# Kernel tuning notes

Measured on AMD Instinct MI355X. Metric: run time of the kernel, lower is better.

The kernel has to match this reference:

```python
import jax, jax.numpy as jnp
import numpy as np

DIN = 256
HID = 512

def setup_inputs() -> dict:
    key = jax.random.key(0)
    ks = jax.random.split(key, 9)
    s_in = 1.0 / np.sqrt(DIN)
    s_h = 1.0 / np.sqrt(HID)
    h = jax.random.normal(ks[0], (32, 1024, DIN), dtype=jnp.float32)
    Wv = jax.random.uniform(ks[1], (HID, DIN), jnp.float32, -s_in, s_in)
    bv = jax.random.uniform(ks[2], (HID,), jnp.float32, -s_in, s_in)
    Wk = jax.random.uniform(ks[3], (HID, DIN), jnp.float32, -s_in, s_in)
    bk = jax.random.uniform(ks[4], (HID,), jnp.float32, -s_in, s_in)
    Wq = jax.random.uniform(ks[5], (HID, DIN), jnp.float32, -s_in, s_in)
    bq = jax.random.uniform(ks[6], (HID,), jnp.float32, -s_in, s_in)
    Wo = jax.random.uniform(ks[7], (DIN, HID), jnp.float32, -s_h, s_h)
    bo = jax.random.uniform(ks[8], (DIN,), jnp.float32, -s_h, s_h)
    return {"h": h, "Wv": Wv, "bv": bv, "Wk": Wk, "bk": bk, "Wq": Wq, "bq": bq, "Wo": Wo, "bo": bo}

def reference(h, Wv, bv, Wk, bk, Wq, bq, Wo, bo):
    # relu-activated Q/K/V projections: [B, N, HID]
    v = jax.nn.relu(jnp.einsum('bnd,hd->bnh', h, Wv) + bv)
    q = jax.nn.relu(jnp.einsum('bnd,hd->bnh', h, Wq) + bq)
    k = jax.nn.relu(jnp.einsum('bnd,hd->bnh', h, Wk) + bk)
    # unscaled attention: [B, N, N]
    att = jax.nn.softmax(jnp.einsum('bnh,bmh->bnm', q, k), axis=2)
    out = jnp.einsum('bnm,bmh->bnh', att, v)          # [B, N, HID]
    out = jax.nn.relu(jnp.einsum('bnh,dh->bnd', out, Wo) + bo)  # [B, N, DIN]
    return out
```

## Files before the change

kernel.cpp:

```cpp
#include <hip/hip_runtime.h>
#include <cstdint>
#include <cstddef>

#define NB    32
#define SEQ   1024
#define DIN   256
#define HID   512
#define MTOT  32768

typedef _Float16 half_t;
typedef _Float16 half8  __attribute__((ext_vector_type(8)));
typedef _Float16 half4v __attribute__((ext_vector_type(4)));
typedef float    f32x4  __attribute__((ext_vector_type(4)));

typedef __attribute__((address_space(1))) const void* gas_ptr;
typedef __attribute__((address_space(3))) void*       las_ptr;

__global__ void cvt_kernel(const float* __restrict__ src, half_t* __restrict__ dst, int n4) {
    int i = blockIdx.x * blockDim.x + threadIdx.x;
    if (i < n4) {
        f32x4 v = ((const f32x4*)src)[i];
        half4v h;
        h[0] = (half_t)v[0]; h[1] = (half_t)v[1]; h[2] = (half_t)v[2]; h[3] = (half_t)v[3];
        ((half4v*)dst)[i] = h;
    }
}

__global__ void pack_bias(const float* __restrict__ bv, const float* __restrict__ bk,
                          const float* __restrict__ bq, float* __restrict__ dst) {
    int t = threadIdx.x;
    if (t < HID) {
        dst[t]         = bv[t];
        dst[HID + t]   = bk[t];
        dst[2*HID + t] = bq[t];
    }
}

template<int MODE>
__global__ __launch_bounds__(256, 2) void gemm_k(
    const half_t* __restrict__ A, long lda, long a_bs,
    const half_t* __restrict__ Bw, long ldb, long b_bs,
    void* __restrict__ Out, long ldo, long o_bs,
    const float* __restrict__ bias,
    int Kdim, half_t* __restrict__ out2)
{
    __shared__ alignas(16) half_t As[128 * 32];
    __shared__ alignas(16) half_t Bs[128 * 32];

    const int t    = threadIdx.x;
    const int lane = t & 63;
    const int wave = t >> 6;
    const int wm   = wave >> 1;
    const int wn   = wave & 1;
    const int lanen = lane & 15;
    const int quad  = lane >> 4;
    const int z     = blockIdx.z;
    const long m0 = (long)blockIdx.x * 128;
    const long n0 = (long)blockIdx.y * 128;

    const half_t* Ab = A  + (long)z * a_bs;
    const half_t* Bb = Bw + (long)z * b_bs;

    f32x4 acc[4][4];
#pragma unroll
    for (int i = 0; i < 4; i++)
#pragma unroll
        for (int j = 0; j < 4; j++)
            acc[i][j] = f32x4{0.f, 0.f, 0.f, 0.f};

    const int c0 = t, c1 = t + 256;
    const int r0 = c0 >> 2, kc0 = c0 & 3;
    const int r1 = c1 >> 2, kc1 = c1 & 3;

    const half_t* gA0 = Ab + (m0 + r0) * lda + kc0 * 8;
    const half_t* gA1 = Ab + (m0 + r1) * lda + kc1 * 8;
    const half_t* gB0 = Bb + (n0 + r0) * ldb + kc0 * 8;
    const half_t* gB1 = Bb + (n0 + r1) * ldb + kc1 * 8;
    half_t* lA0 = &As[c0 * 8];
    half_t* lA1 = &As[c1 * 8];
    half_t* lB0 = &Bs[c0 * 8];
    half_t* lB1 = &Bs[c1 * 8];

    int aoff[4], boff[4];
#pragma unroll
    for (int i = 0; i < 4; i++) aoff[i] = (wm * 64 + i * 16 + lanen) * 32 + quad * 8;
#pragma unroll
    for (int j = 0; j < 4; j++) boff[j] = (wn * 64 + j * 16 + lanen) * 32 + quad * 8;

    for (int k0 = 0; k0 < Kdim; k0 += 32) {
        __builtin_amdgcn_global_load_lds((gas_ptr)(gA0 + k0), (las_ptr)lA0, 16, 0, 0);
        __builtin_amdgcn_global_load_lds((gas_ptr)(gA1 + k0), (las_ptr)lA1, 16, 0, 0);
        __builtin_amdgcn_global_load_lds((gas_ptr)(gB0 + k0), (las_ptr)lB0, 16, 0, 0);
        __builtin_amdgcn_global_load_lds((gas_ptr)(gB1 + k0), (las_ptr)lB1, 16, 0, 0);
        __syncthreads();

        half8 af[4], bf[4];
#pragma unroll
        for (int i = 0; i < 4; i++) af[i] = *(const half8*)&As[aoff[i]];
#pragma unroll
        for (int j = 0; j < 4; j++) bf[j] = *(const half8*)&Bs[boff[j]];
#pragma unroll
        for (int i = 0; i < 4; i++)
#pragma unroll
            for (int j = 0; j < 4; j++)
                acc[i][j] = __builtin_amdgcn_mfma_f32_16x16x32_f16(af[i], bf[j], acc[i][j], 0, 0, 0);
        __syncthreads();
    }

#pragma unroll
    for (int i = 0; i < 4; i++) {
        long mrow = m0 + wm * 64 + i * 16 + quad * 4;
#pragma unroll
        for (int j = 0; j < 4; j++) {
            long gn = n0 + wn * 64 + j * 16 + lanen;
            f32x4 v = acc[i][j];
            if (MODE == 0) {
                float bb = bias[z * HID + gn];
                half_t h0 = (half_t)fmaxf(v[0] + bb, 0.f);
                half_t h1 = (half_t)fmaxf(v[1] + bb, 0.f);
                half_t h2 = (half_t)fmaxf(v[2] + bb, 0.f);
                half_t h3 = (half_t)fmaxf(v[3] + bb, 0.f);
                if (z == 0) {
                    long bidx = mrow >> 10;
                    long pos  = mrow & 1023;
                    half4v pk; pk[0] = h0; pk[1] = h1; pk[2] = h2; pk[3] = h3;
                    *(half4v*)(out2 + ((bidx * HID + gn) << 10) + pos) = pk;
                } else {
                    half_t* o = (half_t*)Out + (long)(z - 1) * o_bs;
                    o[(mrow + 0) * ldo + gn] = h0;
                    o[(mrow + 1) * ldo + gn] = h1;
                    o[(mrow + 2) * ldo + gn] = h2;
                    o[(mrow + 3) * ldo + gn] = h3;
                }
            } else {
                float* o = (float*)Out;
                float bb = bias[gn];
#pragma unroll
                for (int r = 0; r < 4; r++) o[(mrow + r) * ldo + gn] = fmaxf(v[r] + bb, 0.f);
            }
        }
    }
}

__global__ __launch_bounds__(256, 2) void se_k(
    const half_t* __restrict__ Q, const half_t* __restrict__ K,
    half_t* __restrict__ E, float* __restrict__ Mstat, float* __restrict__ Lstat)
{
    __shared__ alignas(16) half_t As[128 * 32];
    __shared__ alignas(16) half_t Bs[128 * 32];
    __shared__ float redM[2][128];
    __shared__ float redL[2][128];

    const int t    = threadIdx.x;
    const int lane = t & 63;
    const int wave = t >> 6;
    const int wm   = wave >> 1;
    const int wn   = wave & 1;
    const int lanen = lane & 15;
    const int quad  = lane >> 4;
    const int z     = blockIdx.z;
    const int kb    = blockIdx.y;
    const long m0 = (long)blockIdx.x * 128;
    const long n0 = (long)kb * 128;

    const half_t* Ab = Q + (long)z * SEQ * HID;
    const half_t* Bb = K + (long)z * SEQ * HID;

    f32x4 acc[4][4];
#pragma unroll
    for (int i = 0; i < 4; i++)
#pragma unroll
        for (int j = 0; j < 4; j++)
            acc[i][j] = f32x4{0.f, 0.f, 0.f, 0.f};

    const int c0 = t, c1 = t + 256;
    const int r0 = c0 >> 2, kc0 = c0 & 3;
    const int r1 = c1 >> 2, kc1 = c1 & 3;

    const half_t* gA0 = Ab + (m0 + r0) * HID + kc0 * 8;
    const half_t* gA1 = Ab + (m0 + r1) * HID + kc1 * 8;
    const half_t* gB0 = Bb + (n0 + r0) * HID + kc0 * 8;
    const half_t* gB1 = Bb + (n0 + r1) * HID + kc1 * 8;
    half_t* lA0 = &As[c0 * 8];
    half_t* lA1 = &As[c1 * 8];
    half_t* lB0 = &Bs[c0 * 8];
    half_t* lB1 = &Bs[c1 * 8];

    int aoff[4], boff[4];
#pragma unroll
    for (int i = 0; i < 4; i++) aoff[i] = (wm * 64 + i * 16 + lanen) * 32 + quad * 8;
#pragma unroll
    for (int j = 0; j < 4; j++) boff[j] = (wn * 64 + j * 16 + lanen) * 32 + quad * 8;

    for (int k0 = 0; k0 < HID; k0 += 32) {
        __builtin_amdgcn_global_load_lds((gas_ptr)(gA0 + k0), (las_ptr)lA0, 16, 0, 0);
        __builtin_amdgcn_global_load_lds((gas_ptr)(gA1 + k0), (las_ptr)lA1, 16, 0, 0);
        __builtin_amdgcn_global_load_lds((gas_ptr)(gB0 + k0), (las_ptr)lB0, 16, 0, 0);
        __builtin_amdgcn_global_load_lds((gas_ptr)(gB1 + k0), (las_ptr)lB1, 16, 0, 0);
        __syncthreads();

        half8 af[4], bf[4];
#pragma unroll
        for (int i = 0; i < 4; i++) af[i] = *(const half8*)&As[aoff[i]];
#pragma unroll
        for (int j = 0; j < 4; j++) bf[j] = *(const half8*)&Bs[boff[j]];
#pragma unroll
        for (int i = 0; i < 4; i++)
#pragma unroll
            for (int j = 0; j < 4; j++)
                acc[i][j] = __builtin_amdgcn_mfma_f32_16x16x32_f16(af[i], bf[j], acc[i][j], 0, 0, 0);
        __syncthreads();
    }

    float rm[4][4];
#pragma unroll
    for (int i = 0; i < 4; i++)
#pragma unroll
        for (int r = 0; r < 4; r++) {
            float v = fmaxf(fmaxf(acc[i][0][r], acc[i][1][r]), fmaxf(acc[i][2][r], acc[i][3][r]));
#pragma unroll
            for (int off = 8; off > 0; off >>= 1)
                v = fmaxf(v, __shfl_xor(v, off, 64));
            rm[i][r] = v;
        }
    if (lanen == 0) {
#pragma unroll
        for (int i = 0; i < 4; i++)
#pragma unroll
            for (int r = 0; r < 4; r++)
                redM[wn][wm * 64 + i * 16 + quad * 4 + r] = rm[i][r];
    }
    __syncthreads();

    float mf[4][4];
#pragma unroll
    for (int i = 0; i < 4; i++)
#pragma unroll
        for (int r = 0; r < 4; r++) {
            int rl = wm * 64 + i * 16 + quad * 4 + r;
            mf[i][r] = fmaxf(redM[0][rl], redM[1][rl]);
        }

    half_t* Eb = E + (long)z * SEQ * SEQ;
    float rs[4][4];
#pragma unroll
    for (int i = 0; i < 4; i++)
#pragma unroll
        for (int r = 0; r < 4; r++) rs[i][r] = 0.f;
#pragma unroll
    for (int i = 0; i < 4; i++) {
        long mrow = m0 + wm * 64 + i * 16 + quad * 4;
#pragma unroll
        for (int j = 0; j < 4; j++) {
            long gn = n0 + wn * 64 + j * 16 + lanen;
#pragma unroll
            for (int r = 0; r < 4; r++) {
                float e = __expf(acc[i][j][r] - mf[i][r]);
                rs[i][r] += e;
                Eb[(mrow + r) * SEQ + gn] = (half_t)e;
            }
        }
    }
#pragma unroll
    for (int i = 0; i < 4; i++)
#pragma unroll
        for (int r = 0; r < 4; r++) {
            float v = rs[i][r];
#pragma unroll
            for (int off = 8; off > 0; off >>= 1)
                v += __shfl_xor(v, off, 64);
            rs[i][r] = v;
        }
    if (lanen == 0) {
#pragma unroll
        for (int i = 0; i < 4; i++)
#pragma unroll
            for (int r = 0; r < 4; r++)
                redL[wn][wm * 64 + i * 16 + quad * 4 + r] = rs[i][r];
    }
    __syncthreads();

    if (t < 128) {
        long sidx = ((long)z * 8 + kb) * SEQ + m0 + t;
        Mstat[sidx] = fmaxf(redM[0][t], redM[1][t]);
        Lstat[sidx] = redL[0][t] + redL[1][t];
    }
}

__global__ __launch_bounds__(256, 2) void pv_k(
    const half_t* __restrict__ E, const half_t* __restrict__ vT,
    const float* __restrict__ Mstat, const float* __restrict__ Lstat,
    half_t* __restrict__ O16)
{
    __shared__ alignas(16) half_t As[128 * 32];
    __shared__ alignas(16) half_t Bs[128 * 32];
    __shared__ float scaleS[8][128];
    __shared__ float invS[128];

    const int t    = threadIdx.x;
    const int lane = t & 63;
    const int wave = t >> 6;
    const int wm   = wave >> 1;
    const int wn   = wave & 1;
    const int lanen = lane & 15;
    const int quad  = lane >> 4;
    const int z     = blockIdx.z;
    const long m0 = (long)blockIdx.x * 128;
    const long h0 = (long)blockIdx.y * 128;

    if (t < 128) {
        float mv[8];
        float M = -1e30f;
#pragma unroll
        for (int kb = 0; kb < 8; kb++) {
            mv[kb] = Mstat[((long)z * 8 + kb) * SEQ + m0 + t];
            M = fmaxf(M, mv[kb]);
        }
        float ls = 0.f;
#pragma unroll
        for (int kb = 0; kb < 8; kb++) {
            float sc = __expf(mv[kb] - M);
            scaleS[kb][t] = sc;
            ls += Lstat[((long)z * 8 + kb) * SEQ + m0 + t] * sc;
        }
        invS[t] = 1.f / ls;
    }
    __syncthreads();

    const half_t* Ab = E  + (long)z * SEQ * SEQ;
    const half_t* Bb = vT + (long)z * HID * SEQ;

    f32x4 acc[4][4];
#pragma unroll
    for (int i = 0; i < 4; i++)
#pragma unroll
        for (int j = 0; j < 4; j++)
            acc[i][j] = f32x4{0.f, 0.f, 0.f, 0.f};

    const int c0 = t, c1 = t + 256;
    const int r0 = c0 >> 2, kc0 = c0 & 3;
    const int r1 = c1 >> 2, kc1 = c1 & 3;

    const half_t* gA0 = Ab + (m0 + r0) * SEQ + kc0 * 8;
    const half_t* gA1 = Ab + (m0 + r1) * SEQ + kc1 * 8;
    const half_t* gB0 = Bb + (h0 + r0) * SEQ + kc0 * 8;
    const half_t* gB1 = Bb + (h0 + r1) * SEQ + kc1 * 8;
    half_t* lA0 = &As[c0 * 8];
    half_t* lA1 = &As[c1 * 8];
    half_t* lB0 = &Bs[c0 * 8];
    half_t* lB1 = &Bs[c1 * 8];

    int aoff[4], boff[4];
#pragma unroll
    for (int i = 0; i < 4; i++) aoff[i] = (wm * 64 + i * 16 + lanen) * 32 + quad * 8;
#pragma unroll
    for (int j = 0; j < 4; j++) boff[j] = (wn * 64 + j * 16 + lanen) * 32 + quad * 8;

    for (int k0 = 0; k0 < SEQ; k0 += 32) {
        __builtin_amdgcn_global_load_lds((gas_ptr)(gA0 + k0), (las_ptr)lA0, 16, 0, 0);
        __builtin_amdgcn_global_load_lds((gas_ptr)(gA1 + k0), (las_ptr)lA1, 16, 0, 0);
        __builtin_amdgcn_global_load_lds((gas_ptr)(gB0 + k0), (las_ptr)lB0, 16, 0, 0);
        __builtin_amdgcn_global_load_lds((gas_ptr)(gB1 + k0), (las_ptr)lB1, 16, 0, 0);
        __syncthreads();

        const int kb = k0 >> 7;
        half8 af[4], bf[4];
#pragma unroll
        for (int i = 0; i < 4; i++) {
            af[i] = *(const half8*)&As[aoff[i]];
            half_t sh = (half_t)scaleS[kb][wm * 64 + i * 16 + lanen];
            af[i] *= sh;
        }
#pragma unroll
        for (int j = 0; j < 4; j++) bf[j] = *(const half8*)&Bs[boff[j]];
#pragma unroll
        for (int i = 0; i < 4; i++)
#pragma unroll
            for (int j = 0; j < 4; j++)
                acc[i][j] = __builtin_amdgcn_mfma_f32_16x16x32_f16(af[i], bf[j], acc[i][j], 0, 0, 0);
        __syncthreads();
    }

    half_t* o = O16 + (long)z * SEQ * HID;
#pragma unroll
    for (int i = 0; i < 4; i++) {
        long mrow = m0 + wm * 64 + i * 16 + quad * 4;
        int rl = wm * 64 + i * 16 + quad * 4;
#pragma unroll
        for (int j = 0; j < 4; j++) {
            long gn = h0 + wn * 64 + j * 16 + lanen;
#pragma unroll
            for (int r = 0; r < 4; r++)
                o[(mrow + r) * HID + gn] = (half_t)(acc[i][j][r] * invS[rl + r]);
        }
    }
}

extern "C" void kernel_launch(void* const* d_in, const int* in_sizes, int n_in,
                              void* d_out, int out_size, void* d_ws, size_t ws_size,
                              hipStream_t stream) {
    const float* h  = (const float*)d_in[0];
    const float* Wv = (const float*)d_in[1];
    const float* bv = (const float*)d_in[2];
    const float* Wk = (const float*)d_in[3];
    const float* bk = (const float*)d_in[4];
    const float* Wq = (const float*)d_in[5];
    const float* bq = (const float*)d_in[6];
    const float* Wo = (const float*)d_in[7];
    const float* bo = (const float*)d_in[8];

    uint8_t* ws = (uint8_t*)d_ws;
    size_t off = 0;
    auto alloc = [&](size_t bytes) { size_t o = off; off += (bytes + 255) & ~(size_t)255; return o; };

    half_t* W16   = (half_t*)(ws + alloc((size_t)3 * HID * DIN * 2));
    half_t* Wo16  = (half_t*)(ws + alloc((size_t)DIN * HID * 2));
    float*  biasq = (float*)(ws + alloc((size_t)3 * HID * 4));
    half_t* k16   = (half_t*)(ws + alloc((size_t)MTOT * HID * 2));
    half_t* q16   = (half_t*)(ws + alloc((size_t)MTOT * HID * 2));
    half_t* vT    = (half_t*)(ws + alloc((size_t)MTOT * HID * 2));
    size_t h16_off = alloc((size_t)MTOT * DIN * 2);
    half_t* h16   = (half_t*)(ws + h16_off);
    half_t* O16 = q16;

    size_t s_avail = ws_size > h16_off ? ws_size - h16_off : 0;
    size_t per_batch = (size_t)SEQ * SEQ * 2 + 2 * 8 * SEQ * 4;
    int GB = (int)(s_avail / per_batch);
    if (GB < 1)  GB = 1;
    if (GB > NB) GB = NB;
    half_t* Ebuf  = (half_t*)(ws + h16_off);
    float*  Mstat = (float*)(ws + h16_off + (size_t)GB * SEQ * SEQ * 2);
    float*  Lstat = Mstat + (size_t)GB * 8 * SEQ;

    cvt_kernel<<<dim3((MTOT * DIN / 4 + 255) / 256), 256, 0, stream>>>(h, h16, MTOT * DIN / 4);
    cvt_kernel<<<dim3((HID * DIN / 4 + 255) / 256), 256, 0, stream>>>(Wv, W16, HID * DIN / 4);
    cvt_kernel<<<dim3((HID * DIN / 4 + 255) / 256), 256, 0, stream>>>(Wk, W16 + HID * DIN, HID * DIN / 4);
    cvt_kernel<<<dim3((HID * DIN / 4 + 255) / 256), 256, 0, stream>>>(Wq, W16 + 2 * HID * DIN, HID * DIN / 4);
    cvt_kernel<<<dim3((DIN * HID / 4 + 255) / 256), 256, 0, stream>>>(Wo, Wo16, DIN * HID / 4);
    pack_bias<<<dim3(1), 512, 0, stream>>>(bv, bk, bq, biasq);

    gemm_k<0><<<dim3(MTOT / 128, HID / 128, 3), 256, 0, stream>>>(
        h16, DIN, 0,
        W16, DIN, (long)HID * DIN,
        (void*)k16, HID, (long)MTOT * HID,
        biasq, DIN, vT);

    for (int g0 = 0; g0 < NB; g0 += GB) {
        int gb = NB - g0 < GB ? NB - g0 : GB;
        se_k<<<dim3(SEQ / 128, SEQ / 128, gb), 256, 0, stream>>>(
            q16 + (size_t)g0 * SEQ * HID,
            k16 + (size_t)g0 * SEQ * HID,
            Ebuf, Mstat, Lstat);
        pv_k<<<dim3(SEQ / 128, HID / 128, gb), 256, 0, stream>>>(
            Ebuf, vT + (size_t)g0 * HID * SEQ,
            Mstat, Lstat,
            O16 + (size_t)g0 * SEQ * HID);
    }

    gemm_k<3><<<dim3(MTOT / 128, DIN / 128, 1), 256, 0, stream>>>(
        O16, HID, 0,
        Wo16, HID, 0,
        d_out, DIN, 0,
        bo, HID, nullptr);

    (void)in_sizes; (void)n_in; (void)out_size;
}
```

Measured before the change: 302.0 us.

## Widen attention tiles to 128x256 and merge weight conversions into one launch

The score-exp kernel and the PV kernel now compute 128x256 output tiles per block instead of 128x128. Each wave holds 4x8 MFMA accumulators, which halves the grid and reloads each A tile half as often. In se_k the cross-wave LDS max/sum reduction is removed: each wave writes its own 128-column partial statistics directly into the existing 8 slots per row. The four weight fp32-to-fp16 conversions are merged into a single launch indexed by blockIdx.y. The larger accumulator arrays raise register pressure and may hurt occupancy under launch_bounds(256,2).

```diff
diff --git a/kernel.cpp b/kernel.cpp
--- a/kernel.cpp
+++ b/kernel.cpp
@@ -23,6 +23,22 @@
         half4v h;
         h[0] = (half_t)v[0]; h[1] = (half_t)v[1]; h[2] = (half_t)v[2]; h[3] = (half_t)v[3];
         ((half4v*)dst)[i] = h;
+    }
+}
+
+__global__ void cvt4_kernel(const float* __restrict__ s0, const float* __restrict__ s1,
+                            const float* __restrict__ s2, const float* __restrict__ s3,
+                            half_t* __restrict__ d0, half_t* __restrict__ d1,
+                            half_t* __restrict__ d2, half_t* __restrict__ d3, int n4) {
+    int y = blockIdx.y;
+    const float* s = y == 0 ? s0 : y == 1 ? s1 : y == 2 ? s2 : s3;
+    half_t*      d = y == 0 ? d0 : y == 1 ? d1 : y == 2 ? d2 : d3;
+    int i = blockIdx.x * blockDim.x + threadIdx.x;
+    if (i < n4) {
+        f32x4 v = ((const f32x4*)s)[i];
+        half4v h;
+        h[0] = (half_t)v[0]; h[1] = (half_t)v[1]; h[2] = (half_t)v[2]; h[3] = (half_t)v[3];
+        ((half4v*)d)[i] = h;
     }
 }
 
@@ -147,155 +163,7 @@
     half_t* __restrict__ E, float* __restrict__ Mstat, float* __restrict__ Lstat)
 {
     __shared__ alignas(16) half_t As[128 * 32];
-    __shared__ alignas(16) half_t Bs[128 * 32];
-    __shared__ float redM[2][128];
-    __shared__ float redL[2][128];
-
-    const int t    = threadIdx.x;
-    const int lane = t & 63;
-    const int wave = t >> 6;
-    const int wm   = wave >> 1;
-    const int wn   = wave & 1;
-    const int lanen = lane & 15;
-    const int quad  = lane >> 4;
-    const int z     = blockIdx.z;
-    const int kb    = blockIdx.y;
-    const long m0 = (long)blockIdx.x * 128;
-    const long n0 = (long)kb * 128;
-
-    const half_t* Ab = Q + (long)z * SEQ * HID;
-    const half_t* Bb = K + (long)z * SEQ * HID;
-
-    f32x4 acc[4][4];
-#pragma unroll
-    for (int i = 0; i < 4; i++)
-#pragma unroll
-        for (int j = 0; j < 4; j++)
-            acc[i][j] = f32x4{0.f, 0.f, 0.f, 0.f};
-
-    const int c0 = t, c1 = t + 256;
-    const int r0 = c0 >> 2, kc0 = c0 & 3;
-    const int r1 = c1 >> 2, kc1 = c1 & 3;
-
-    const half_t* gA0 = Ab + (m0 + r0) * HID + kc0 * 8;
-    const half_t* gA1 = Ab + (m0 + r1) * HID + kc1 * 8;
-    const half_t* gB0 = Bb + (n0 + r0) * HID + kc0 * 8;
-    const half_t* gB1 = Bb + (n0 + r1) * HID + kc1 * 8;
-    half_t* lA0 = &As[c0 * 8];
-    half_t* lA1 = &As[c1 * 8];
-    half_t* lB0 = &Bs[c0 * 8];
-    half_t* lB1 = &Bs[c1 * 8];
-
-    int aoff[4], boff[4];
-#pragma unroll
-    for (int i = 0; i < 4; i++) aoff[i] = (wm * 64 + i * 16 + lanen) * 32 + quad * 8;
-#pragma unroll
-    for (int j = 0; j < 4; j++) boff[j] = (wn * 64 + j * 16 + lanen) * 32 + quad * 8;
-
-    for (int k0 = 0; k0 < HID; k0 += 32) {
-        __builtin_amdgcn_global_load_lds((gas_ptr)(gA0 + k0), (las_ptr)lA0, 16, 0, 0);
-        __builtin_amdgcn_global_load_lds((gas_ptr)(gA1 + k0), (las_ptr)lA1, 16, 0, 0);
-        __builtin_amdgcn_global_load_lds((gas_ptr)(gB0 + k0), (las_ptr)lB0, 16, 0, 0);
-        __builtin_amdgcn_global_load_lds((gas_ptr)(gB1 + k0), (las_ptr)lB1, 16, 0, 0);
-        __syncthreads();
-
-        half8 af[4], bf[4];
-#pragma unroll
-        for (int i = 0; i < 4; i++) af[i] = *(const half8*)&As[aoff[i]];
-#pragma unroll
-        for (int j = 0; j < 4; j++) bf[j] = *(const half8*)&Bs[boff[j]];
-#pragma unroll
-        for (int i = 0; i < 4; i++)
-#pragma unroll
-            for (int j = 0; j < 4; j++)
-                acc[i][j] = __builtin_amdgcn_mfma_f32_16x16x32_f16(af[i], bf[j], acc[i][j], 0, 0, 0);
-        __syncthreads();
-    }
-
-    float rm[4][4];
-#pragma unroll
-    for (int i = 0; i < 4; i++)
-#pragma unroll
-        for (int r = 0; r < 4; r++) {
-            float v = fmaxf(fmaxf(acc[i][0][r], acc[i][1][r]), fmaxf(acc[i][2][r], acc[i][3][r]));
-#pragma unroll
-            for (int off = 8; off > 0; off >>= 1)
-                v = fmaxf(v, __shfl_xor(v, off, 64));
-            rm[i][r] = v;
-        }
-    if (lanen == 0) {
-#pragma unroll
-        for (int i = 0; i < 4; i++)
-#pragma unroll
-            for (int r = 0; r < 4; r++)
-                redM[wn][wm * 64 + i * 16 + quad * 4 + r] = rm[i][r];
-    }
-    __syncthreads();
-
-    float mf[4][4];
-#pragma unroll
-    for (int i = 0; i < 4; i++)
-#pragma unroll
-        for (int r = 0; r < 4; r++) {
-            int rl = wm * 64 + i * 16 + quad * 4 + r;
-            mf[i][r] = fmaxf(redM[0][rl], redM[1][rl]);
-        }
-
-    half_t* Eb = E + (long)z * SEQ * SEQ;
-    float rs[4][4];
-#pragma unroll
-    for (int i = 0; i < 4; i++)
-#pragma unroll
-        for (int r = 0; r < 4; r++) rs[i][r] = 0.f;
-#pragma unroll
-    for (int i = 0; i < 4; i++) {
-        long mrow = m0 + wm * 64 + i * 16 + quad * 4;
-#pragma unroll
-        for (int j = 0; j < 4; j++) {
-            long gn = n0 + wn * 64 + j * 16 + lanen;
-#pragma unroll
-            for (int r = 0; r < 4; r++) {
-                float e = __expf(acc[i][j][r] - mf[i][r]);
-                rs[i][r] += e;
-                Eb[(mrow + r) * SEQ + gn] = (half_t)e;
-            }
-        }
-    }
-#pragma unroll
-    for (int i = 0; i < 4; i++)
-#pragma unroll
-        for (int r = 0; r < 4; r++) {
-            float v = rs[i][r];
-#pragma unroll
-            for (int off = 8; off > 0; off >>= 1)
-                v += __shfl_xor(v, off, 64);
-            rs[i][r] = v;
-        }
-    if (lanen == 0) {
-#pragma unroll
-        for (int i = 0; i < 4; i++)
-#pragma unroll
-            for (int r = 0; r < 4; r++)
-                redL[wn][wm * 64 + i * 16 + quad * 4 + r] = rs[i][r];
-    }
-    __syncthreads();
-
-    if (t < 128) {
-        long sidx = ((long)z * 8 + kb) * SEQ + m0 + t;
-        Mstat[sidx] = fmaxf(redM[0][t], redM[1][t]);
-        Lstat[sidx] = redL[0][t] + redL[1][t];
-    }
-}
-
-__global__ __launch_bounds__(256, 2) void pv_k(
-    const half_t* __restrict__ E, const half_t* __restrict__ vT,
-    const float* __restrict__ Mstat, const float* __restrict__ Lstat,
-    half_t* __restrict__ O16)
-{
-    __shared__ alignas(16) half_t As[128 * 32];
-    __shared__ alignas(16) half_t Bs[128 * 32];
-    __shared__ float scaleS[8][128];
-    __shared__ float invS[128];
+    __shared__ alignas(16) half_t Bs[256 * 32];
 
     const int t    = threadIdx.x;
     const int lane = t & 63;
@@ -306,7 +174,138 @@
     const int quad  = lane >> 4;
     const int z     = blockIdx.z;
     const long m0 = (long)blockIdx.x * 128;
-    const long h0 = (long)blockIdx.y * 128;
+    const long n0 = (long)blockIdx.y * 256;
+
+    const half_t* Ab = Q + (long)z * SEQ * HID;
+    const half_t* Bb = K + (long)z * SEQ * HID;
+
+    f32x4 acc[4][8];
+#pragma unroll
+    for (int i = 0; i < 4; i++)
+#pragma unroll
+        for (int j = 0; j < 8; j++)
+            acc[i][j] = f32x4{0.f, 0.f, 0.f, 0.f};
+
+    const half_t* gA[2]; half_t* lA[2];
+    const half_t* gB[4]; half_t* lB[4];
+#pragma unroll
+    for (int s = 0; s < 2; s++) {
+        int c = t + 256 * s;
+        gA[s] = Ab + (m0 + (c >> 2)) * HID + (c & 3) * 8;
+        lA[s] = &As[c * 8];
+    }
+#pragma unroll
+    for (int s = 0; s < 4; s++) {
+        int c = t + 256 * s;
+        gB[s] = Bb + (n0 + (c >> 2)) * HID + (c & 3) * 8;
+        lB[s] = &Bs[c * 8];
+    }
+
+    int aoff[4], boff[8];
+#pragma unroll
+    for (int i = 0; i < 4; i++) aoff[i] = (wm * 64 + i * 16 + lanen) * 32 + quad * 8;
+#pragma unroll
+    for (int j = 0; j < 8; j++) boff[j] = (wn * 128 + j * 16 + lanen) * 32 + quad * 8;
+
+    for (int k0 = 0; k0 < HID; k0 += 32) {
+#pragma unroll
+        for (int s = 0; s < 2; s++)
+            __builtin_amdgcn_global_load_lds((gas_ptr)(gA[s] + k0), (las_ptr)lA[s], 16, 0, 0);
+#pragma unroll
+        for (int s = 0; s < 4; s++)
+            __builtin_amdgcn_global_load_lds((gas_ptr)(gB[s] + k0), (las_ptr)lB[s], 16, 0, 0);
+        __syncthreads();
+
+        half8 af[4], bf[8];
+#pragma unroll
+        for (int i = 0; i < 4; i++) af[i] = *(const half8*)&As[aoff[i]];
+#pragma unroll
+        for (int j = 0; j < 8; j++) bf[j] = *(const half8*)&Bs[boff[j]];
+#pragma unroll
+        for (int i = 0; i < 4; i++)
+#pragma unroll
+            for (int j = 0; j < 8; j++)
+                acc[i][j] = __builtin_amdgcn_mfma_f32_16x16x32_f16(af[i], bf[j], acc[i][j], 0, 0, 0);
+        __syncthreads();
+    }
+
+    float mf[4][4];
+#pragma unroll
+    for (int i = 0; i < 4; i++)
+#pragma unroll
+        for (int r = 0; r < 4; r++) {
+            float v = acc[i][0][r];
+#pragma unroll
+            for (int j = 1; j < 8; j++) v = fmaxf(v, acc[i][j][r]);
+#pragma unroll
+            for (int off = 8; off > 0; off >>= 1)
+                v = fmaxf(v, __shfl_xor(v, off, 64));
+            mf[i][r] = v;
+        }
+
+    half_t* Eb = E + (long)z * SEQ * SEQ;
+    float rs[4][4];
+#pragma unroll
+    for (int i = 0; i < 4; i++)
+#pragma unroll
+        for (int r = 0; r < 4; r++) rs[i][r] = 0.f;
+#pragma unroll
+    for (int i = 0; i < 4; i++) {
+        long mrow = m0 + wm * 64 + i * 16 + quad * 4;
+#pragma unroll
+        for (int j = 0; j < 8; j++) {
+            long gn = n0 + wn * 128 + j * 16 + lanen;
+#pragma unroll
+            for (int r = 0; r < 4; r++) {
+                float e = __expf(acc[i][j][r] - mf[i][r]);
+                rs[i][r] += e;
+                Eb[(mrow + r) * SEQ + gn] = (half_t)e;
+            }
+        }
+    }
+#pragma unroll
+    for (int i = 0; i < 4; i++)
+#pragma unroll
+        for (int r = 0; r < 4; r++) {
+            float v = rs[i][r];
+#pragma unroll
+            for (int off = 8; off > 0; off >>= 1)
+                v += __shfl_xor(v, off, 64);
+            rs[i][r] = v;
+        }
+
+    if (lanen == 0) {
+        long base = ((long)z * 8 + blockIdx.y * 2 + wn) * SEQ + m0 + wm * 64;
+#pragma unroll
+        for (int i = 0; i < 4; i++)
+#pragma unroll
+            for (int r = 0; r < 4; r++) {
+                Mstat[base + i * 16 + quad * 4 + r] = mf[i][r];
+                Lstat[base + i * 16 + quad * 4 + r] = rs[i][r];
+            }
+    }
+}
+
+__global__ __launch_bounds__(256, 2) void pv_k(
+    const half_t* __restrict__ E, const half_t* __restrict__ vT,
+    const float* __restrict__ Mstat, const float* __restrict__ Lstat,
+    half_t* __restrict__ O16)
+{
+    __shared__ alignas(16) half_t As[128 * 32];
+    __shared__ alignas(16) half_t Bs[256 * 32];
+    __shared__ float scaleS[8][128];
+    __shared__ float invS[128];
+
+    const int t    = threadIdx.x;
+    const int lane = t & 63;
+    const int wave = t >> 6;
+    const int wm   = wave >> 1;
+    const int wn   = wave & 1;
+    const int lanen = lane & 15;
+    const int quad  = lane >> 4;
+    const int z     = blockIdx.z;
+    const long m0 = (long)blockIdx.x * 128;
+    const long h0 = (long)blockIdx.y * 256;
 
     if (t < 128) {
         float mv[8];
@@ -330,41 +329,45 @@
     const half_t* Ab = E  + (long)z * SEQ * SEQ;
     const half_t* Bb = vT + (long)z * HID * SEQ;
 
-    f32x4 acc[4][4];
-#pragma unroll
-    for (int i = 0; i < 4; i++)
-#pragma unroll
-        for (int j = 0; j < 4; j++)
+    f32x4 acc[4][8];
+#pragma unroll
+    for (int i = 0; i < 4; i++)
+#pragma unroll
+        for (int j = 0; j < 8; j++)
             acc[i][j] = f32x4{0.f, 0.f, 0.f, 0.f};
 
-    const int c0 = t, c1 = t + 256;
-    const int r0 = c0 >> 2, kc0 = c0 & 3;
-    const int r1 = c1 >> 2, kc1 = c1 & 3;
-
-    const half_t* gA0 = Ab + (m0 + r0) * SEQ + kc0 * 8;
-    const half_t* gA1 = Ab + (m0 + r1) * SEQ + kc1 * 8;
-    const half_t* gB0 = Bb + (h0 + r0) * SEQ + kc0 * 8;
-    const half_t* gB1 = Bb + (h0 + r1) * SEQ + kc1 * 8;
-    half_t* lA0 = &As[c0 * 8];
-    half_t* lA1 = &As[c1 * 8];
-    half_t* lB0 = &Bs[c0 * 8];
-    half_t* lB1 = &Bs[c1 * 8];
-
-    int aoff[4], boff[4];
+    const half_t* gA[2]; half_t* lA[2];
+    const half_t* gB[4]; half_t* lB[4];
+#pragma unroll
+    for (int s = 0; s < 2; s++) {
+        int c = t + 256 * s;
+        gA[s] = Ab + (m0 + (c >> 2)) * SEQ + (c & 3) * 8;
+        lA[s] = &As[c * 8];
+    }
+#pragma unroll
+    for (int s = 0; s < 4; s++) {
+        int c = t + 256 * s;
+        gB[s] = Bb + (h0 + (c >> 2)) * SEQ + (c & 3) * 8;
+        lB[s] = &Bs[c * 8];
+    }
+
+    int aoff[4], boff[8];
 #pragma unroll
     for (int i = 0; i < 4; i++) aoff[i] = (wm * 64 + i * 16 + lanen) * 32 + quad * 8;
 #pragma unroll
-    for (int j = 0; j < 4; j++) boff[j] = (wn * 64 + j * 16 + lanen) * 32 + quad * 8;
+    for (int j = 0; j < 8; j++) boff[j] = (wn * 128 + j * 16 + lanen) * 32 + quad * 8;
 
     for (int k0 = 0; k0 < SEQ; k0 += 32) {
-        __builtin_amdgcn_global_load_lds((gas_ptr)(gA0 + k0), (las_ptr)lA0, 16, 0, 0);
-        __builtin_amdgcn_global_load_lds((gas_ptr)(gA1 + k0), (las_ptr)lA1, 16, 0, 0);
-        __builtin_amdgcn_global_load_lds((gas_ptr)(gB0 + k0), (las_ptr)lB0, 16, 0, 0);
-        __builtin_amdgcn_global_load_lds((gas_ptr)(gB1 + k0), (las_ptr)lB1, 16, 0, 0);
+#pragma unroll
+        for (int s = 0; s < 2; s++)
+            __builtin_amdgcn_global_load_lds((gas_ptr)(gA[s] + k0), (las_ptr)lA[s], 16, 0, 0);
+#pragma unroll
+        for (int s = 0; s < 4; s++)
+            __builtin_amdgcn_global_load_lds((gas_ptr)(gB[s] + k0), (las_ptr)lB[s], 16, 0, 0);
         __syncthreads();
 
         const int kb = k0 >> 7;
-        half8 af[4], bf[4];
+        half8 af[4], bf[8];
 #pragma unroll
         for (int i = 0; i < 4; i++) {
             af[i] = *(const half8*)&As[aoff[i]];
@@ -372,11 +375,11 @@
             af[i] *= sh;
         }
 #pragma unroll
-        for (int j = 0; j < 4; j++) bf[j] = *(const half8*)&Bs[boff[j]];
+        for (int j = 0; j < 8; j++) bf[j] = *(const half8*)&Bs[boff[j]];
 #pragma unroll
         for (int i = 0; i < 4; i++)
 #pragma unroll
-            for (int j = 0; j < 4; j++)
+            for (int j = 0; j < 8; j++)
                 acc[i][j] = __builtin_amdgcn_mfma_f32_16x16x32_f16(af[i], bf[j], acc[i][j], 0, 0, 0);
         __syncthreads();
     }
@@ -387,8 +390,8 @@
         long mrow = m0 + wm * 64 + i * 16 + quad * 4;
         int rl = wm * 64 + i * 16 + quad * 4;
 #pragma unroll
-        for (int j = 0; j < 4; j++) {
-            long gn = h0 + wn * 64 + j * 16 + lanen;
+        for (int j = 0; j < 8; j++) {
+            long gn = h0 + wn * 128 + j * 16 + lanen;
 #pragma unroll
             for (int r = 0; r < 4; r++)
                 o[(mrow + r) * HID + gn] = (half_t)(acc[i][j][r] * invS[rl + r]);
@@ -433,10 +436,8 @@
     float*  Lstat = Mstat + (size_t)GB * 8 * SEQ;
 
     cvt_kernel<<<dim3((MTOT * DIN / 4 + 255) / 256), 256, 0, stream>>>(h, h16, MTOT * DIN / 4);
-    cvt_kernel<<<dim3((HID * DIN / 4 + 255) / 256), 256, 0, stream>>>(Wv, W16, HID * DIN / 4);
-    cvt_kernel<<<dim3((HID * DIN / 4 + 255) / 256), 256, 0, stream>>>(Wk, W16 + HID * DIN, HID * DIN / 4);
-    cvt_kernel<<<dim3((HID * DIN / 4 + 255) / 256), 256, 0, stream>>>(Wq, W16 + 2 * HID * DIN, HID * DIN / 4);
-    cvt_kernel<<<dim3((DIN * HID / 4 + 255) / 256), 256, 0, stream>>>(Wo, Wo16, DIN * HID / 4);
+    cvt4_kernel<<<dim3((HID * DIN / 4 + 255) / 256, 4), 256, 0, stream>>>(
+        Wv, Wk, Wq, Wo, W16, W16 + HID * DIN, W16 + 2 * HID * DIN, Wo16, HID * DIN / 4);
     pack_bias<<<dim3(1), 512, 0, stream>>>(bv, bk, bq, biasq);
 
     gemm_k<0><<<dim3(MTOT / 128, HID / 128, 3), 256, 0, stream>>>(
@@ -447,11 +448,11 @@
 
     for (int g0 = 0; g0 < NB; g0 += GB) {
         int gb = NB - g0 < GB ? NB - g0 : GB;
-        se_k<<<dim3(SEQ / 128, SEQ / 128, gb), 256, 0, stream>>>(
+        se_k<<<dim3(SEQ / 128, SEQ / 256, gb), 256, 0, stream>>>(
             q16 + (size_t)g0 * SEQ * HID,
             k16 + (size_t)g0 * SEQ * HID,
             Ebuf, Mstat, Lstat);
-        pv_k<<<dim3(SEQ / 128, HID / 128, gb), 256, 0, stream>>>(
+        pv_k<<<dim3(SEQ / 128, HID / 256, gb), 256, 0, stream>>>(
             Ebuf, vT + (size_t)g0 * HID * SEQ,
             Mstat, Lstat,
             O16 + (size_t)g0 * SEQ * HID);
```

Result: faster. 290.8 us (-3.7%).
